# Optimization experiments

Measured on AMD Instinct MI355X. Metric: run time of the kernel, lower is better.

## Reference

```python
import jax, jax.numpy as jnp
import numpy as np

B, T, C, H, HS = 2, 2048, 1024, 16, 64


def setup_inputs() -> dict:
    key = jax.random.key(0)
    ks = jax.random.split(key, 7)
    x = jax.random.normal(ks[0], (B, T, C), dtype=jnp.float32)
    # causal mask, broadcast over batch (True = attend)
    attention_mask = jnp.broadcast_to(jnp.tril(jnp.ones((T, T), dtype=bool)), (B, T, T))
    s = 1.0 / np.sqrt(C)
    wq = jax.random.normal(ks[1], (H, C, HS), dtype=jnp.float32) * s   # per-head query Linear (no bias)
    wk = jax.random.normal(ks[2], (H, C, HS), dtype=jnp.float32) * s
    wv = jax.random.normal(ks[3], (H, C, HS), dtype=jnp.float32) * s
    wproj = jax.random.normal(ks[4], (H * HS, C), dtype=jnp.float32) * (1.0 / np.sqrt(H * HS))
    bproj = jnp.zeros((C,), dtype=jnp.float32)
    return {"x": x, "attention_mask": attention_mask,
            "wq": wq, "wk": wk, "wv": wv, "wproj": wproj, "bproj": bproj}


def reference(x, attention_mask, wq, wk, wv, wproj, bproj):
    # per-head projections: [B,H,T,HS]
    q = jnp.einsum('btc,hcd->bhtd', x, wq)
    k = jnp.einsum('btc,hcd->bhtd', x, wk)
    v = jnp.einsum('btc,hcd->bhtd', x, wv)
    scale = 1.0 / jnp.sqrt(jnp.asarray(HS, dtype=x.dtype))
    wei = jnp.einsum('bhtd,bhsd->bhts', q, k) * scale          # [B,H,T,T]
    wei = jnp.where(attention_mask[:, None, :, :], wei, -jnp.inf)
    wei = jax.nn.softmax(wei, axis=-1)
    out = jnp.einsum('bhts,bhsd->bhtd', wei, v)                 # [B,H,T,HS]
    out = out.transpose(0, 2, 1, 3).reshape(B, T, H * HS)       # concat heads
    return out @ wproj + bproj                                  # [B,T,C]
```

## Files before the change

kernel.cpp:

```cpp
#include <hip/hip_runtime.h>
#include <math.h>

typedef float f32x4 __attribute__((ext_vector_type(4)));
typedef __bf16 bf16x8 __attribute__((ext_vector_type(8)));
typedef unsigned short u16x8 __attribute__((ext_vector_type(8)));
typedef unsigned short u16x4 __attribute__((ext_vector_type(4)));

#define DEV static __device__ __forceinline__

DEV unsigned short f2bf(float f) {
    unsigned int u = __builtin_bit_cast(unsigned int, f);
    u += 0x7fffu + ((u >> 16) & 1u);
    return (unsigned short)(u >> 16);
}

#define GLD16(gp, lp) __builtin_amdgcn_global_load_lds( \
    (__attribute__((address_space(1))) void*)(gp),      \
    (__attribute__((address_space(3))) void*)(lp), 16, 0, 0)

#define WAITBAR(N) asm volatile("s_waitcnt vmcnt(" #N ")\n\ts_barrier" ::: "memory")
#define BARRIER()  asm volatile("s_barrier" ::: "memory")

__global__ __launch_bounds__(256) void k_prep(const float* __restrict__ x,
                                              const float* __restrict__ wq,
                                              const float* __restrict__ wk,
                                              const float* __restrict__ wv,
                                              const float* __restrict__ wproj,
                                              unsigned short* __restrict__ xb,
                                              unsigned short* __restrict__ WqkvT,
                                              unsigned short* __restrict__ WprojT) {
    const int bid = blockIdx.x, tid = threadIdx.x;
    if (bid < 2048) {
        int i = bid * 256 + tid;
        const float4* p = (const float4*)(x + (size_t)i * 8);
        float4 a = p[0], b = p[1];
        u16x8 o;
        o[0] = f2bf(a.x); o[1] = f2bf(a.y); o[2] = f2bf(a.z); o[3] = f2bf(a.w);
        o[4] = f2bf(b.x); o[5] = f2bf(b.y); o[6] = f2bf(b.z); o[7] = f2bf(b.w);
        *(u16x8*)(xb + (size_t)i * 8) = o;
        return;
    }
    __shared__ unsigned short t[64][68];
    if (bid < 2816) {
        int zb = bid - 2048;
        int z = zb >> 4, wsel = z >> 4, zz = z & 15;
        const float* src = (wsel == 0 ? wq : wsel == 1 ? wk : wv) + (size_t)zz * 65536;
        int r0 = (zb & 15) * 64;
#pragma unroll
        for (int it = 0; it < 4; ++it) {
            int r = (tid >> 4) + it * 16;
            int c4 = (tid & 15) * 4;
            float4 v = *(const float4*)&src[(size_t)(r0 + r) * 64 + c4];
            t[c4 + 0][r] = f2bf(v.x);
            t[c4 + 1][r] = f2bf(v.y);
            t[c4 + 2][r] = f2bf(v.z);
            t[c4 + 3][r] = f2bf(v.w);
        }
        __syncthreads();
#pragma unroll
        for (int it = 0; it < 4; ++it) {
            int c = (tid >> 4) + it * 16;
            int r4 = (tid & 15) * 4;
            u16x4 o;
            o[0] = t[c][r4 + 0]; o[1] = t[c][r4 + 1];
            o[2] = t[c][r4 + 2]; o[3] = t[c][r4 + 3];
            int row = wsel * 1024 + zz * 64 + c;
            *(u16x4*)&WqkvT[(size_t)row * 1024 + r0 + r4] = o;
        }
    } else {
        int zb = bid - 2816;
        int r0 = (zb & 15) * 64, c0 = (zb >> 4) * 64;
#pragma unroll
        for (int it = 0; it < 4; ++it) {
            int r = (tid >> 4) + it * 16;
            int c4 = (tid & 15) * 4;
            float4 v = *(const float4*)&wproj[(size_t)(r0 + r) * 1024 + c0 + c4];
            t[c4 + 0][r] = f2bf(v.x);
            t[c4 + 1][r] = f2bf(v.y);
            t[c4 + 2][r] = f2bf(v.z);
            t[c4 + 3][r] = f2bf(v.w);
        }
        __syncthreads();
#pragma unroll
        for (int it = 0; it < 4; ++it) {
            int c = (tid >> 4) + it * 16;
            int r4 = (tid & 15) * 4;
            u16x4 o;
            o[0] = t[c][r4 + 0]; o[1] = t[c][r4 + 1];
            o[2] = t[c][r4 + 2]; o[3] = t[c][r4 + 3];
            *(u16x4*)&WprojT[(size_t)(c0 + c) * 1024 + r0 + r4] = o;
        }
    }
}

template <int STAGE, int M_REP, int NB, int SUPM, int SUPN>
__global__ __launch_bounds__(256) void k_gemm(const unsigned short* __restrict__ A,
                                              const unsigned short* __restrict__ Bt,
                                              int Kd,
                                              float* __restrict__ outF,
                                              const float* __restrict__ bias,
                                              unsigned short* __restrict__ Qb,
                                              unsigned short* __restrict__ Kb,
                                              unsigned short* __restrict__ Vt) {
    constexpr int BM = M_REP * 32;
    __shared__ unsigned short As[2][BM * 64] __attribute__((aligned(16)));
    __shared__ unsigned short Bs[2][128 * 64] __attribute__((aligned(16)));
    const int tid = threadIdx.x, l = tid & 63, w = tid >> 6;
    constexpr int BN_CH = NB / SUPN;
    const int orig = blockIdx.x;
    const int xcd = orig & 7, sdx = orig >> 3;
    const int bm = (xcd / BN_CH) * SUPM + (sdx % SUPM);
    const int bn = (xcd % BN_CH) * SUPN + (sdx / SUPM);
    const int wr = w >> 1, wc = w & 1;
    const int g = l >> 4, q = l & 15;
    f32x4 acc[M_REP][4] = {};
    const unsigned short* gA = A + (size_t)(bm * BM + w * 8 + (l >> 3)) * Kd + (l & 7) * 8;
    const unsigned short* gB = Bt + (size_t)(bn * 128 + w * 8 + (l >> 3)) * Kd + (l & 7) * 8;

#define GSTAGE(buf, k0) do {                                                  \
        _Pragma("unroll")                                                     \
        for (int it = 0; it < M_REP; ++it)                                    \
            GLD16(gA + (size_t)(it * 32) * Kd + (k0), &As[buf][(it * 32 + w * 8) * 64]); \
        _Pragma("unroll")                                                     \
        for (int it = 0; it < 4; ++it)                                        \
            GLD16(gB + (size_t)(it * 32) * Kd + (k0), &Bs[buf][(it * 32 + w * 8) * 64]); \
    } while (0)

    const int nt = Kd >> 6;
    GSTAGE(0, 0);
    int cur = 0;
    for (int t = 0; t < nt; ++t) {
        if (t + 1 < nt) {
            GSTAGE(cur ^ 1, (t + 1) << 6);
            if constexpr (M_REP == 4) WAITBAR(8); else WAITBAR(6);
        } else {
            WAITBAR(0);
        }
#pragma unroll
        for (int ks = 0; ks < 2; ++ks) {
            bf16x8 af[M_REP], bfr[4];
#pragma unroll
            for (int mi = 0; mi < M_REP; ++mi)
                af[mi] = *(const bf16x8*)&As[cur][(wr * (M_REP * 16) + mi * 16 + q) * 64 + ks * 32 + g * 8];
#pragma unroll
            for (int ni = 0; ni < 4; ++ni)
                bfr[ni] = *(const bf16x8*)&Bs[cur][(wc * 64 + ni * 16 + q) * 64 + ks * 32 + g * 8];
#pragma unroll
            for (int mi = 0; mi < M_REP; ++mi)
#pragma unroll
                for (int ni = 0; ni < 4; ++ni)
                    acc[mi][ni] = __builtin_amdgcn_mfma_f32_16x16x32_bf16(
                        af[mi], bfr[ni], acc[mi][ni], 0, 0, 0);
        }
        BARRIER();
        cur ^= 1;
    }
#undef GSTAGE
#pragma unroll
    for (int mi = 0; mi < M_REP; ++mi)
#pragma unroll
        for (int ni = 0; ni < 4; ++ni)
#pragma unroll
            for (int r = 0; r < 4; ++r) {
                float c = acc[mi][ni][r];
                int m = bm * BM + wr * (M_REP * 16) + mi * 16 + g * 4 + r;
                int n = bn * 128 + wc * 64 + ni * 16 + q;
                if (STAGE == 1) {
                    int b = m >> 11, t = m & 2047;
                    int proj = n >> 10, rr = n & 1023, h = rr >> 6, d = rr & 63;
                    int bh = b * 16 + h;
                    if (proj == 0)
                        Qb[((size_t)bh * 2048 + t) * 64 + d] = f2bf(c * 0.18033688011112042f);
                    else if (proj == 1)
                        Kb[((size_t)bh * 2048 + t) * 64 + d] = f2bf(c);
                    else
                        Vt[((size_t)bh * 64 + d) * 2048 + t] = f2bf(c);
                } else {
                    outF[(size_t)m * 1024 + n] = c + bias[n];
                }
            }
}

__global__ __launch_bounds__(256) void k_attn(const unsigned short* __restrict__ Qb,
                                              const unsigned short* __restrict__ Kb,
                                              const unsigned short* __restrict__ Vt,
                                              unsigned short* __restrict__ att) {
    __shared__ unsigned short Ks[2][2][4096] __attribute__((aligned(16)));
    __shared__ unsigned short Vs[2][2][4096] __attribute__((aligned(16)));
    __shared__ unsigned short P[4][16][72];
    const int tid = threadIdx.x, l = tid & 63, w = tid >> 6;
    const int pj = blockIdx.x, bh = blockIdx.y;
    const int b = bh >> 4, h = bh & 15;
    const int ql = l & 15, g = l >> 4;
    const unsigned short* Qp = Qb + (size_t)bh * 2048 * 64;
    const unsigned short* Kp = Kb + (size_t)bh * 2048 * 64;
    const unsigned short* Vp = Vt + (size_t)bh * 64 * 2048;

    const int sr0 = w * 16 + (l >> 3);
    const int sch = (l & 7) ^ (l >> 3);
    const unsigned short* gK0 = Kp + (size_t)sr0 * 64 + sch * 8;
    const unsigned short* gK1 = gK0 + 8 * 64;
    const unsigned short* gV0 = Vp + (size_t)sr0 * 2048 + sch * 8;
    const unsigned short* gV1 = gV0 + 8 * 2048;

#define ATT_STAGE(buf, kvb) do {                                                  \
        GLD16(gK0 + (size_t)(kvb) * 64, &Ks[buf][0][(w * 16) * 64]);              \
        GLD16(gK1 + (size_t)(kvb) * 64, &Ks[buf][0][(w * 16 + 8) * 64]);          \
        GLD16(gK0 + (size_t)((kvb) + 64) * 64, &Ks[buf][1][(w * 16) * 64]);       \
        GLD16(gK1 + (size_t)((kvb) + 64) * 64, &Ks[buf][1][(w * 16 + 8) * 64]);   \
        GLD16(gV0 + (kvb), &Vs[buf][0][(w * 16) * 64]);                           \
        GLD16(gV1 + (kvb), &Vs[buf][0][(w * 16 + 8) * 64]);                       \
        GLD16(gV0 + (kvb) + 64, &Vs[buf][1][(w * 16) * 64]);                      \
        GLD16(gV1 + (kvb) + 64, &Vs[buf][1][(w * 16 + 8) * 64]);                  \
    } while (0)

    for (int ph = 0; ph < 2; ++ph) {
        const int qt = ph ? (31 - pj) : pj;
        const int qg = qt * 64 + w * 16 + ql;
        const int minqg = qt * 64 + w * 16;
        const int nkv2 = (qt + 2) >> 1;

        bf16x8 qf0 = *(const bf16x8*)(Qp + (size_t)qg * 64 + g * 8);
        bf16x8 qf1 = *(const bf16x8*)(Qp + (size_t)qg * 64 + 32 + g * 8);
        f32x4 ot[4] = {};
        float mrun = -1e30f, lsum = 0.f;

        ATT_STAGE(0, 0);
        int cur = 0;

        for (int kb = 0; kb < nkv2; ++kb) {
            if (kb + 1 < nkv2) {
                ATT_STAGE(cur ^ 1, (kb + 1) * 128);
                WAITBAR(8);
            } else {
                WAITBAR(0);
            }
#pragma unroll
            for (int sub = 0; sub < 2; ++sub) {
                const int kvb = kb * 128 + sub * 64;
                const unsigned short* Kt = &Ks[cur][sub][0];
                const unsigned short* Vtl = &Vs[cur][sub][0];
                f32x4 st[4] = {};
                bf16x8 kf0[4], kf1[4];
#pragma unroll
                for (int f = 0; f < 4; ++f) {
                    int rk = f * 16 + ql, sw = rk & 7;
                    kf0[f] = *(const bf16x8*)&Kt[rk * 64 + ((g ^ sw) * 8)];
                    kf1[f] = *(const bf16x8*)&Kt[rk * 64 + (((g + 4) ^ sw) * 8)];
                }
                __builtin_amdgcn_s_setprio(1);
#pragma unroll
                for (int f = 0; f < 4; ++f) {
                    st[f] = __builtin_amdgcn_mfma_f32_16x16x32_bf16(kf0[f], qf0, st[f], 0, 0, 0);
                    st[f] = __builtin_amdgcn_mfma_f32_16x16x32_bf16(kf1[f], qf1, st[f], 0, 0, 0);
                }
                __builtin_amdgcn_s_setprio(0);
                if (kvb + 63 > minqg) {
#pragma unroll
                    for (int f = 0; f < 4; ++f)
#pragma unroll
                        for (int r = 0; r < 4; ++r)
                            if (kvb + f * 16 + g * 4 + r > qg) st[f][r] = -1e30f;
                }
                float pmax = -1e30f;
#pragma unroll
                for (int f = 0; f < 4; ++f)
#pragma unroll
                    for (int r = 0; r < 4; ++r) pmax = fmaxf(pmax, st[f][r]);
                if (!__all(pmax <= mrun + 8.f)) {
                    float pm = fmaxf(pmax, __shfl_xor(pmax, 16));
                    pm = fmaxf(pm, __shfl_xor(pm, 32));
                    float mnew = fmaxf(mrun, pm);
                    float corr = __builtin_amdgcn_exp2f(mrun - mnew);
                    lsum *= corr;
#pragma unroll
                    for (int f = 0; f < 4; ++f) ot[f] *= corr;
                    mrun = mnew;
                }
                float psum = 0.f;
#pragma unroll
                for (int f = 0; f < 4; ++f) {
                    u16x4 pk;
#pragma unroll
                    for (int r = 0; r < 4; ++r) {
                        float p = __builtin_amdgcn_exp2f(st[f][r] - mrun);
                        psum += p;
                        pk[r] = f2bf(p);
                    }
                    *(u16x4*)&P[w][ql][f * 16 + g * 4] = pk;
                }
                lsum += psum;
                asm volatile("s_waitcnt lgkmcnt(0)" ::: "memory");
#pragma unroll
                for (int dc = 0; dc < 2; ++dc) {
                    bf16x8 pf = *(const bf16x8*)&P[w][ql][dc * 32 + g * 8];
                    __builtin_amdgcn_s_setprio(1);
#pragma unroll
                    for (int f = 0; f < 4; ++f) {
                        int rv = f * 16 + ql, sw = rv & 7;
                        bf16x8 vf = *(const bf16x8*)&Vtl[rv * 64 + (((dc * 4 + g) ^ sw) * 8)];
                        ot[f] = __builtin_amdgcn_mfma_f32_16x16x32_bf16(vf, pf, ot[f], 0, 0, 0);
                    }
                    __builtin_amdgcn_s_setprio(0);
                }
            }
            BARRIER();
            cur ^= 1;
        }
        lsum += __shfl_xor(lsum, 16);
        lsum += __shfl_xor(lsum, 32);
        float inv = 1.f / lsum;
        unsigned short* ap = att + ((size_t)(b * 2048 + qg)) * 1024 + h * 64;
#pragma unroll
        for (int f = 0; f < 4; ++f) {
            u16x4 o;
#pragma unroll
            for (int r = 0; r < 4; ++r) o[r] = f2bf(ot[f][r] * inv);
            *(u16x4*)&ap[f * 16 + g * 4] = o;
        }
    }
#undef ATT_STAGE
}

extern "C" void kernel_launch(void* const* d_in, const int* in_sizes, int n_in,
                              void* d_out, int out_size, void* d_ws, size_t ws_size,
                              hipStream_t stream) {
    const float* x = (const float*)d_in[0];
    const float* wq = (const float*)d_in[2];
    const float* wk = (const float*)d_in[3];
    const float* wv = (const float*)d_in[4];
    const float* wproj = (const float*)d_in[5];
    const float* bproj = (const float*)d_in[6];
    float* out = (float*)d_out;

    char* ws = (char*)d_ws;
    unsigned short* xb     = (unsigned short*)(ws);
    unsigned short* WqkvT  = (unsigned short*)(ws + (8u << 20));
    unsigned short* WprojT = (unsigned short*)(ws + (14u << 20));
    unsigned short* Qb     = (unsigned short*)(ws + (16u << 20));
    unsigned short* Kb     = (unsigned short*)(ws + (24u << 20));
    unsigned short* Vt     = (unsigned short*)(ws + (32u << 20));
    unsigned short* att    = xb;

    k_prep<<<3072, 256, 0, stream>>>(x, wq, wk, wv, wproj, xb, WqkvT, WprojT);
    k_gemm<1, 2, 24, 16, 12><<<1536, 256, 0, stream>>>(xb, WqkvT, 1024, nullptr, nullptr, Qb, Kb, Vt);
    k_attn<<<dim3(16, 32), 256, 0, stream>>>(Qb, Kb, Vt, att);
    k_gemm<3, 2, 8, 16, 4><<<512, 256, 0, stream>>>(att, WprojT, 1024, out, bproj, nullptr, nullptr, nullptr);
}
```

Measured before the change: 133.8 us.

## Use 512-thread 128x128-tile GEMM kernel for QKV projection

Adds a new GEMM kernel with 8 waves per block and a 128x128 output tile, each wave computing a 64x32 subtile. It replaces the 64x128-tile, 256-thread kernel for the QKV projection, halving the number of blocks and increasing operand reuse per tile loaded into shared memory. The trade-off is fewer blocks to fill the GPU (768) and more registers and LDS per block, which may lower occupancy.

```diff
diff --git a/kernel.cpp b/kernel.cpp
--- a/kernel.cpp
+++ b/kernel.cpp
@@ -93,6 +93,92 @@
     }
 }
 
+template <int STAGE, int NB, int SUPM, int SUPN>
+__global__ __launch_bounds__(512) void k_gemm8(const unsigned short* __restrict__ A,
+                                               const unsigned short* __restrict__ Bt,
+                                               int Kd,
+                                               float* __restrict__ outF,
+                                               const float* __restrict__ bias,
+                                               unsigned short* __restrict__ Qb,
+                                               unsigned short* __restrict__ Kb,
+                                               unsigned short* __restrict__ Vt) {
+    __shared__ unsigned short As[2][128 * 64] __attribute__((aligned(16)));
+    __shared__ unsigned short Bs[2][128 * 64] __attribute__((aligned(16)));
+    const int tid = threadIdx.x, l = tid & 63, w = tid >> 6;
+    constexpr int BN_CH = NB / SUPN;
+    const int orig = blockIdx.x;
+    const int xcd = orig & 7, sdx = orig >> 3;
+    const int bm = (xcd / BN_CH) * SUPM + (sdx % SUPM);
+    const int bn = (xcd % BN_CH) * SUPN + (sdx / SUPM);
+    const int wm = w >> 2, wn = w & 3;
+    const int g = l >> 4, q = l & 15;
+    f32x4 acc[4][2] = {};
+    const unsigned short* gA = A + (size_t)(bm * 128 + w * 8 + (l >> 3)) * Kd + (l & 7) * 8;
+    const unsigned short* gB = Bt + (size_t)(bn * 128 + w * 8 + (l >> 3)) * Kd + (l & 7) * 8;
+
+#define GSTAGE8(buf, k0) do {                                                 \
+        _Pragma("unroll")                                                     \
+        for (int it = 0; it < 2; ++it) {                                      \
+            GLD16(gA + (size_t)(it * 64) * Kd + (k0), &As[buf][(it * 64 + w * 8) * 64]); \
+            GLD16(gB + (size_t)(it * 64) * Kd + (k0), &Bs[buf][(it * 64 + w * 8) * 64]); \
+        }                                                                     \
+    } while (0)
+
+    const int nt = Kd >> 6;
+    GSTAGE8(0, 0);
+    int cur = 0;
+    for (int t = 0; t < nt; ++t) {
+        if (t + 1 < nt) {
+            GSTAGE8(cur ^ 1, (t + 1) << 6);
+            WAITBAR(4);
+        } else {
+            WAITBAR(0);
+        }
+#pragma unroll
+        for (int ks = 0; ks < 2; ++ks) {
+            bf16x8 af[4], bfr[2];
+#pragma unroll
+            for (int mi = 0; mi < 4; ++mi)
+                af[mi] = *(const bf16x8*)&As[cur][(wm * 64 + mi * 16 + q) * 64 + ks * 32 + g * 8];
+#pragma unroll
+            for (int ni = 0; ni < 2; ++ni)
+                bfr[ni] = *(const bf16x8*)&Bs[cur][(wn * 32 + ni * 16 + q) * 64 + ks * 32 + g * 8];
+#pragma unroll
+            for (int mi = 0; mi < 4; ++mi)
+#pragma unroll
+                for (int ni = 0; ni < 2; ++ni)
+                    acc[mi][ni] = __builtin_amdgcn_mfma_f32_16x16x32_bf16(
+                        af[mi], bfr[ni], acc[mi][ni], 0, 0, 0);
+        }
+        BARRIER();
+        cur ^= 1;
+    }
+#undef GSTAGE8
+#pragma unroll
+    for (int mi = 0; mi < 4; ++mi)
+#pragma unroll
+        for (int ni = 0; ni < 2; ++ni)
+#pragma unroll
+            for (int r = 0; r < 4; ++r) {
+                float c = acc[mi][ni][r];
+                int m = bm * 128 + wm * 64 + mi * 16 + g * 4 + r;
+                int n = bn * 128 + wn * 32 + ni * 16 + q;
+                if (STAGE == 1) {
+                    int b = m >> 11, t = m & 2047;
+                    int proj = n >> 10, rr = n & 1023, h = rr >> 6, d = rr & 63;
+                    int bh = b * 16 + h;
+                    if (proj == 0)
+                        Qb[((size_t)bh * 2048 + t) * 64 + d] = f2bf(c * 0.18033688011112042f);
+                    else if (proj == 1)
+                        Kb[((size_t)bh * 2048 + t) * 64 + d] = f2bf(c);
+                    else
+                        Vt[((size_t)bh * 64 + d) * 2048 + t] = f2bf(c);
+                } else {
+                    outF[(size_t)m * 1024 + n] = c + bias[n];
+                }
+            }
+}
+
 template <int STAGE, int M_REP, int NB, int SUPM, int SUPN>
 __global__ __launch_bounds__(256) void k_gemm(const unsigned short* __restrict__ A,
                                               const unsigned short* __restrict__ Bt,
@@ -343,7 +429,7 @@
     unsigned short* att    = xb;
 
     k_prep<<<3072, 256, 0, stream>>>(x, wq, wk, wv, wproj, xb, WqkvT, WprojT);
-    k_gemm<1, 2, 24, 16, 12><<<1536, 256, 0, stream>>>(xb, WqkvT, 1024, nullptr, nullptr, Qb, Kb, Vt);
+    k_gemm8<1, 24, 8, 12><<<768, 512, 0, stream>>>(xb, WqkvT, 1024, nullptr, nullptr, Qb, Kb, Vt);
     k_attn<<<dim3(16, 32), 256, 0, stream>>>(Qb, Kb, Vt, att);
     k_gemm<3, 2, 8, 16, 4><<<512, 256, 0, stream>>>(att, WprojT, 1024, out, bproj, nullptr, nullptr, nullptr);
 }
```

New measurement: 136.4 us. Within noise of the previous version (+1.9%).
